# Performance work log

Hardware: AMD Instinct MI355X
Metric: run time of the kernel (lower is better)

## Reference

```python
import jax, jax.numpy as jnp
import numpy as np

NQ = 10          # qubits
NT = 32          # tokens (LCU terms)
DM = 512         # d_model
DEG = 2          # qsvt degree
B = 128          # batch
NPQC = 4 * NQ    # params per PQC application
DIM = 2 ** NQ    # statevector dimension


def ansatz14_spec(q, layers=1):
    spec = []
    for _ in range(layers):
        spec += [('ry', (i,)) for i in range(q)]
        spec += [('crx', (i, (i + 1) % q)) for i in range(q - 1, -1, -1)]
        spec += [('ry', (i,)) for i in range(q)]
        spec += [('crx', (i, (i - 1) % q)) for i in [q - 1] + list(range(q - 1))]
    return spec

SPEC = ansatz14_spec(NQ, 1)


def _gate_ry(theta):
    h = theta * 0.5
    c = jnp.cos(h)
    s = jnp.sin(h)
    m = jnp.stack([jnp.stack([c, -s], -1), jnp.stack([s, c], -1)], -2)
    return m.astype(jnp.complex64)  # (N,2,2)


def _gate_rx(theta):
    h = theta * 0.5
    c = jnp.cos(h).astype(jnp.complex64)
    s = (-1j) * jnp.sin(h).astype(jnp.complex64)
    return jnp.stack([jnp.stack([c, s], -1), jnp.stack([s, c], -1)], -2)


def _apply_1q(state, mats, wire, q):
    # state: (N, 2^q) complex; mats: (N,2,2); wire 0 is most significant bit
    N = state.shape[0]
    a = 2 ** wire
    bdim = 2 ** (q - wire - 1)
    s = state.reshape(N, a, 2, bdim)
    return jnp.einsum('nij,najb->naib', mats, s).reshape(N, 2 ** q)


def _apply_crx(state, theta, c, t, q):
    # controlled-RX: control wire c, target wire t
    N = state.shape[0]
    st = state.reshape((N,) + (2,) * q)
    ax = 1 + c
    s0 = jnp.take(st, 0, axis=ax)   # control = 0 branch: untouched
    s1 = jnp.take(st, 1, axis=ax)   # control = 1 branch: apply RX on target
    tp = t if t < c else t - 1      # target wire position after removing control axis
    s1n = _apply_1q(s1.reshape(N, -1), _gate_rx(theta), tp, q - 1).reshape(s1.shape)
    return jnp.stack([s0, s1n], axis=ax).reshape(N, 2 ** q)


def _apply_pqc(state, params, q):
    # params: (N, NPQC); fixed small gate list -> Python loop is fine
    for k, (fn, w) in enumerate(SPEC):
        th = params[:, k]
        if fn == 'ry':
            state = _apply_1q(state, _gate_ry(th), w[0], q)
        else:
            state = _apply_crx(state, th, w[0], w[1], q)
    return state


def _apply_lcu(states, params, lcu):
    # states: (B, DIM) complex; params: (B, L, NPQC); lcu: (B, L) complex
    Bn, L = lcu.shape
    rep = jnp.repeat(states, L, axis=0)                    # (B*L, DIM)
    st = _apply_pqc(rep, params.reshape(Bn * L, NPQC), NQ)
    return jnp.einsum('bld,bl->bd', st.reshape(Bn, L, DIM), lcu)


def _measure_xyz(state, q):
    # Pauli expectations per wire: order [X_0..X_{q-1}, Y_0.., Z_0..]
    N = state.shape[0]
    xs, ys, zs = [], [], []
    for w in range(q):
        s = state.reshape(N, 2 ** w, 2, -1)
        a0, a1 = s[:, :, 0, :], s[:, :, 1, :]
        cross = jnp.sum(jnp.conj(a0) * a1, axis=(1, 2))
        xs.append(2.0 * jnp.real(cross))
        ys.append(2.0 * jnp.imag(cross))
        zs.append(jnp.sum(jnp.abs(a0) ** 2 - jnp.abs(a1) ** 2, axis=(1, 2)))
    return jnp.stack(xs + ys + zs, axis=1).astype(jnp.float32)  # (B, 3q)


def reference(tokens_emb, W, b, lcu_re, lcu_im, qsvt_coeffs, ff_params):
    Bn, L, D = tokens_emb.shape
    L = min(L, NT)
    pqc_params = tokens_emb[:, :L] @ W.T + b               # (B, L, NPQC)
    lcu = (lcu_re + 1j * lcu_im).astype(jnp.complex64)[:L]
    lcu = lcu / jnp.sum(jnp.abs(lcu))
    lcu_b = jnp.broadcast_to(lcu[None], (Bn, L))
    init = jnp.zeros((Bn, DIM), jnp.complex64).at[:, 0].set(1.0)
    acc = qsvt_coeffs[0].astype(jnp.complex64) * init
    mono = init
    for k in range(1, DEG + 1):
        mono = _apply_lcu(mono, pqc_params, lcu_b)
        acc = acc + qsvt_coeffs[k].astype(jnp.complex64) * mono
    state = acc / jnp.sum(jnp.abs(qsvt_coeffs))
    state = state / jnp.linalg.norm(state, axis=-1, keepdims=True)
    ffp = jnp.broadcast_to(ff_params[None], (Bn, NPQC))
    state = _apply_pqc(state, ffp, NQ)
    return _measure_xyz(state, NQ)


def setup_inputs():
    key = jax.random.key(0)
    ks = jax.random.split(key, 7)
    return {
        'tokens_emb': jax.random.normal(ks[0], (B, NT, DM), jnp.float32),
        'W': jax.random.normal(ks[1], (NPQC, DM), jnp.float32) * 0.05,
        'b': jax.random.normal(ks[2], (NPQC,), jnp.float32),
        'lcu_re': jax.random.normal(ks[3], (NT,), jnp.float32),
        'lcu_im': jax.random.normal(ks[4], (NT,), jnp.float32),
        'qsvt_coeffs': jax.random.normal(ks[5], (DEG + 1,), jnp.float32),
        'ff_params': jax.random.normal(ks[6], (NPQC,), jnp.float32),
    }
```

## Files before the change

### kernel.cpp

```cpp
#include <hip/hip_runtime.h>
#include <hip/hip_bf16.h>


#define NQ   10
#define NT   32
#define DM   512
#define BATCH 128
#define NPQC 40
#define DIM  1024
#define NROWS (BATCH * NT)
#define PSTRIDE (BATCH * DIM)

typedef float v2f __attribute__((ext_vector_type(2)));

#define WAITLDS asm volatile("s_waitcnt lgkmcnt(0)" ::: "memory")

__device__ __forceinline__ v2f Jrot(v2f v) {
  return __builtin_shufflevector(v, -v, 1, 2);
}
__device__ __forceinline__ v2f Jc(v2f v) {
  return __builtin_shufflevector(-v, v, 1, 2);
}


template<int B>
__device__ __forceinline__ void g_ry(v2f (&a)[16], float c, float s) {
  static_assert(B >= 6, "RY targets must be register bits");
  constexpr int m = 1 << (B - 6);
#pragma unroll
  for (int r = 0; r < 16; ++r) {
    if (!(r & m)) {
      int r1 = r | m;
      v2f a0 = a[r], a1 = a[r1];
      a[r]  = c * a0 - s * a1;
      a[r1] = s * a0 + c * a1;
    }
  }
}

template<int BC, int BT>
__device__ __forceinline__ void g_crx(v2f (&a)[16], int lane, float c, float s) {
  static_assert(BT >= 6, "CRX targets must be register bits");
  constexpr int m = 1 << (BT - 6);
  bool lane_ok = (BC >= 6) || ((lane >> BC) & 1);
  float ce = lane_ok ? c : 1.f;
  float se = lane_ok ? s : 0.f;
#pragma unroll
  for (int r = 0; r < 16; ++r) {
    if (!(r & m)) {
      if constexpr (BC >= 6) { if (!((r >> (BC - 6)) & 1)) continue; }
      int r1 = r | m;
      v2f a0 = a[r], a1 = a[r1];
      a[r]  = ce * a0 + se * Jrot(a1);
      a[r1] = ce * a1 + se * Jrot(a0);
    }
  }
}

template<int L0, int L1, int L2, int L3>
__device__ __forceinline__ void remap(v2f (&a)[16], v2f* __restrict__ slab,
                                      int lane) {
  constexpr int LM = (1 << L0) | (1 << L1) | (1 << L2) | (1 << L3);
#pragma unroll
  for (int r = 0; r < 16; ++r) {
    int f = 0;
    if (L0 < 4 && (r & 1)) f |= 1 << L0;
    if (L1 < 4 && (r & 2)) f |= 1 << L1;
    if (L2 < 4 && (r & 4)) f |= 1 << L2;
    if (L3 < 4 && (r & 8)) f |= 1 << L3;
    slab[r * 64 + (lane ^ f)] = a[r];
  }
  WAITLDS;
  int la = lane & ~LM & 63;
  la |= ((lane >> L0) & 1) << 6;
  la |= ((lane >> L1) & 1) << 7;
  la |= ((lane >> L2) & 1) << 8;
  la |= ((lane >> L3) & 1) << 9;
  if (L0 < 4) la |= ((lane >> L0) & 1) << L0;
  if (L1 < 4) la |= ((lane >> L1) & 1) << L1;
  if (L2 < 4) la |= ((lane >> L2) & 1) << L2;
  if (L3 < 4) la |= ((lane >> L3) & 1) << L3;
#pragma unroll
  for (int r = 0; r < 16; ++r) {
    int rc = ((r & 1) ? (1 << L0) : 0) | ((r & 2) ? (1 << L1) : 0)
           | ((r & 4) ? (1 << L2) : 0) | ((r & 8) ? (1 << L3) : 0);
    a[r] = slab[la ^ rc];
  }
}

template<bool SKIP_HEAD>
__device__ __forceinline__ void apply_pqc_phased(v2f (&a)[16],
    const float2* __restrict__ cs, v2f* __restrict__ slab, int lane) {
#define RYt(B, t)      g_ry<B>(a, t.x, t.y);
#define CXt(BC, BT, t) g_crx<BC, BT>(a, lane, t.x, t.y);
  float2 t10 = cs[10], t11 = cs[11], t12 = cs[12];
  if constexpr (!SKIP_HEAD) {
    float2 t0 = cs[0], t1 = cs[1], t2 = cs[2], t3 = cs[3];
    float2 t4 = cs[4], t5 = cs[5], t6 = cs[6], t7 = cs[7];
    float2 t8 = cs[8], t9 = cs[9];
    RYt(9,t0) RYt(8,t1) RYt(7,t2) RYt(6,t3)
    remap<5,4,3,2>(a, slab, lane);
    RYt(6,t4) RYt(7,t5) RYt(8,t6) RYt(9,t7)
    remap<1,0,2,3>(a, slab, lane);
    RYt(6,t8) RYt(7,t9)
  }
  CXt(7,8,t10) CXt(6,7,t11) CXt(3,6,t12)
  float2 t13 = cs[13], t14 = cs[14], t15 = cs[15], t16 = cs[16];
  remap<1,0,2,3>(a, slab, lane);
  CXt(8,9,t13) CXt(7,8,t14) CXt(6,7,t15) CXt(5,6,t16)
  float2 t17 = cs[17], t18 = cs[18], t19 = cs[19];
  float2 t20 = cs[20], t21 = cs[21], t22 = cs[22], t23 = cs[23];
  remap<2,3,4,5>(a, slab, lane);
  CXt(8,9,t17) CXt(7,8,t18) CXt(6,7,t19)
  RYt(6,t20) RYt(7,t21) RYt(8,t22) RYt(9,t23)
  float2 t24 = cs[24], t25 = cs[25], t26 = cs[26], t27 = cs[27];
  remap<2,3,4,5>(a, slab, lane);
  RYt(6,t24) RYt(7,t25) RYt(8,t26) RYt(9,t27)
  float2 t28 = cs[28], t29 = cs[29];
  float2 t30 = cs[30], t31 = cs[31], t32 = cs[32], t33 = cs[33];
  remap<1,0,2,3>(a, slab, lane);
  RYt(6,t28) RYt(7,t29)
  CXt(7,6,t30) CXt(8,7,t31) CXt(9,8,t32) CXt(4,9,t33)
  float2 t34 = cs[34], t35 = cs[35], t36 = cs[36], t37 = cs[37];
  remap<4,5,1,0>(a, slab, lane);
  CXt(7,6,t34) CXt(8,7,t35) CXt(9,8,t36) CXt(2,9,t37)
  float2 t38 = cs[38], t39 = cs[39];
  remap<2,3,4,5>(a, slab, lane);
  CXt(7,6,t38) CXt(8,7,t39)
#undef RYt
#undef CXt
}

__device__ __forceinline__ int p8_lane_canon(int lane) {
  return (((lane >> 1) & 1) << 9) | ((lane & 1) << 8) | (((lane >> 2) & 1) << 7)
       | (((lane >> 3) & 1) << 6) | (((lane >> 4) & 1) << 5) | (((lane >> 5) & 1) << 4);
}

__device__ __forceinline__ void stagger(int key) {
  int s = key & 3;
  if (s & 1) __builtin_amdgcn_s_sleep(1);
  if (s & 2) __builtin_amdgcn_s_sleep(2);
}

__global__ __launch_bounds__(256) void params_kernel(
    const float* __restrict__ emb, const float* __restrict__ W,
    const float* __restrict__ bias,
    const float* __restrict__ lcu_re, const float* __restrict__ lcu_im,
    const float* __restrict__ ffp,
    float2* __restrict__ cs, float2* __restrict__ ffcs, float2* __restrict__ lcu) {
  int blk = blockIdx.x;
  int tid = threadIdx.x;
  if (blk == 256) {
    if (tid < NPQC) {
      float h = 0.5f * ffp[tid];
      ffcs[tid] = make_float2(cosf(h), sinf(h));
    }
    if (tid == 64) {
      float ssum = 0.f;
      for (int i = 0; i < NT; ++i) {
        float re = lcu_re[i], im = lcu_im[i];
        ssum += sqrtf(re * re + im * im);
      }
      float inv = 1.f / ssum;
      for (int i = 0; i < NT; ++i)
        lcu[i] = make_float2(lcu_re[i] * inv, lcu_im[i] * inv);
    }
    return;
  }

  __shared__ float Asl[16 * 516];
  int row0 = blk * 16;

  const float4* eg = (const float4*)(emb + (size_t)row0 * DM);
#pragma unroll
  for (int i = 0; i < 8; ++i) {
    int e = tid + i * 256;
    int r = e >> 7, k4 = e & 127;
    float4 v = eg[e];
    *(float4*)&Asl[r * 516 + k4 * 4] = v;
  }
  __syncthreads();

  int kq = tid >> 6;
  int lane = tid & 63;
  int rg = lane >> 3;
  int cg = lane & 7;

  const float* Ar0 = &Asl[(2 * rg) * 516 + kq * 128];
  const float* Ar1 = Ar0 + 516;
  const float* Bg  = W + (size_t)(5 * cg) * DM + kq * 128;

  float acc[2][5] = {};
#pragma unroll 4
  for (int k = 0; k < 128; k += 4) {
    float4 a0 = *(const float4*)(Ar0 + k);
    float4 a1 = *(const float4*)(Ar1 + k);
#pragma unroll
    for (int j = 0; j < 5; ++j) {
      float4 b = *(const float4*)(Bg + j * DM + k);
      acc[0][j] += a0.x * b.x + a0.y * b.y + a0.z * b.z + a0.w * b.w;
      acc[1][j] += a1.x * b.x + a1.y * b.y + a1.z * b.z + a1.w * b.w;
    }
  }

  __syncthreads();
  float* red = Asl;
#pragma unroll
  for (int i = 0; i < 2; ++i)
#pragma unroll
    for (int j = 0; j < 5; ++j)
      red[kq * 644 + (2 * rg + i) * 40 + 5 * cg + j] = acc[i][j];
  __syncthreads();

  for (int o = tid; o < 640; o += 256) {
    float v = bias[o % 40] + red[o] + red[644 + o] + red[1288 + o] + red[1932 + o];
    float h = 0.5f * v;
    cs[(size_t)blk * 640 + o] = make_float2(cosf(h), sinf(h));
  }
}

template<bool FIRST>
__global__ __launch_bounds__(256) void pqc_step(
    const float2* __restrict__ cs, const float2* __restrict__ lcu,
    const v2f* __restrict__ src, v2f* __restrict__ dst) {
  __shared__ v2f slabs[4][1024];
  int lane = threadIdx.x & 63;
  int wvu = __builtin_amdgcn_readfirstlane(threadIdx.x >> 6);
  int blk = blockIdx.x;
  stagger(blk + wvu);
  int b = blk >> 3, qq = blk & 7;
  int l = qq * 4 + wvu;
  const float2* csrow = cs + (size_t)(b * NT + l) * NPQC;
  v2f* slab = slabs[wvu];

  v2f a[16];
  if constexpr (FIRST) {
    float2 f5 = csrow[5], f4 = csrow[4], f6 = csrow[6], f7 = csrow[7];
    float2 f2 = csrow[2], f3 = csrow[3];
    float2 f8 = csrow[8], f9 = csrow[9], f0 = csrow[0], f1 = csrow[1];
    float lp = ((lane & 1) ? f5.y : f5.x);
    lp *= ((lane & 2) ? f4.y : f4.x);
    lp *= ((lane & 4) ? f6.y : f6.x);
    lp *= ((lane & 8) ? f7.y : f7.x);
    lp *= ((lane & 16) ? f2.y : f2.x);
    lp *= ((lane & 32) ? f3.y : f3.x);
#pragma unroll
    for (int r = 0; r < 16; ++r) {
      float rp = ((r & 1) ? f8.y : f8.x) * ((r & 2) ? f9.y : f9.x)
               * ((r & 4) ? f0.y : f0.x) * ((r & 8) ? f1.y : f1.x);
      a[r].x = lp * rp;
      a[r].y = 0.f;
    }
  } else {
    const v2f* s = src + (size_t)b * DIM;
#pragma unroll
    for (int r = 0; r < 16; ++r) a[r] = s[r * 64 + lane];
  }

  apply_pqc_phased<FIRST>(a, csrow, slab, lane);

  float2 w = lcu[l];
  int pl = p8_lane_canon(lane);
  pl ^= (pl >> 5);
#pragma unroll
  for (int r = 0; r < 16; ++r) {
    int rc = ((r & 1) << 3) | ((r & 2) << 1) | ((r & 4) >> 1) | ((r & 8) >> 3);
    slab[pl ^ rc] = w.x * a[r] + w.y * Jc(a[r]);
  }
  __syncthreads();

  v2f* dst_b = dst + (size_t)(qq * BATCH + b) * DIM;
#pragma unroll
  for (int i = 0; i < 4; ++i) {
    int n = threadIdx.x + i * 256;
    int ph = n ^ (n >> 5);
    v2f sum = slabs[0][ph] + slabs[1][ph] + slabs[2][ph] + slabs[3][ph];
    dst_b[n] = sum;
  }
}


__global__ __launch_bounds__(256) void reduce_slices(v2f* __restrict__ buf) {
  int n = blockIdx.x * 256 + threadIdx.x;
  v2f acc = buf[n];
#pragma unroll
  for (int q = 1; q < 8; ++q) acc += buf[n + q * PSTRIDE];
  buf[n] = acc;
}

__global__ __launch_bounds__(256) void final_reduce(
    const v2f* __restrict__ red1, v2f* __restrict__ part2,
    const float* __restrict__ qsvt) {
  __shared__ float rbuf[4];
  int b = blockIdx.x, tid = threadIdx.x;
  int lane = tid & 63, wv = tid >> 6;
  float q0 = qsvt[0], q1 = qsvt[1], q2 = qsvt[2];
  const v2f* r1 = red1 + (size_t)b * DIM;
  v2f* p2 = part2 + (size_t)b * DIM;

  v2f vals[4];
  float nn = 0.f;
#pragma unroll
  for (int i = 0; i < 4; ++i) {
    int n = tid + i * 256;
    v2f m2 = p2[n];
#pragma unroll
    for (int q = 1; q < 8; ++q) m2 += p2[n + q * PSTRIDE];
    v2f v = q1 * r1[n] + q2 * m2;
    if (n == 0) v.x += q0;
    vals[i] = v;
    nn += v.x * v.x + v.y * v.y;
  }
#pragma unroll
  for (int o = 1; o < 64; o <<= 1) nn += __shfl_xor(nn, o);
  if (lane == 0) rbuf[wv] = nn;
  __syncthreads();
  float inv = 1.f / sqrtf(rbuf[0] + rbuf[1] + rbuf[2] + rbuf[3]);
#pragma unroll
  for (int i = 0; i < 4; ++i) p2[tid + i * 256] = vals[i] * inv;
}

__global__ __launch_bounds__(64, 1) void final_pqc(
    const v2f* __restrict__ state, const float2* __restrict__ ffcs,
    float* __restrict__ out) {
  __shared__ v2f st[1024];
  __shared__ float2 ang[40];
  __shared__ float tb[30 * 65];
  int lane = threadIdx.x;
  int b = blockIdx.x;

  const v2f* s = state + (size_t)b * DIM;
#pragma unroll
  for (int r = 0; r < 16; ++r) {
    int n = r * 64 + lane;
    st[n ^ (n >> 5)] = s[n];
  }
  if (lane < NPQC) ang[lane] = ffcs[lane];
  WAITLDS;

#pragma unroll 1
  for (int k = 0; k < NPQC; ++k) {
    int isCrx, c, t;
    if (k < 10)      { isCrx = 0; t = k;      c = 0; }
    else if (k < 20) { int i = 19 - k; isCrx = 1; c = i; t = (i == 9) ? 0 : i + 1; }
    else if (k < 30) { isCrx = 0; t = k - 20; c = 0; }
    else             { int i = (k == 30) ? 9 : k - 31; isCrx = 1; c = i; t = (i == 0) ? 9 : i - 1; }
    int m  = 1 << (9 - t);
    int cb = 9 - c;
    float2 th = ang[k];
    float cg = th.x, sg = th.y;

    v2f a0[8], a1[8];
    int j0[8], j1[8], en[8];
#pragma unroll
    for (int p = 0; p < 8; ++p) {
      int q  = p * 64 + lane;
      int i0 = ((q & ~(m - 1)) << 1) | (q & (m - 1));
      int i1 = i0 | m;
      j0[p] = i0 ^ (i0 >> 5);
      j1[p] = i1 ^ (i1 >> 5);
      en[p] = (i0 >> cb) & 1;
      a0[p] = st[j0[p]];
      a1[p] = st[j1[p]];
    }
    WAITLDS;
#pragma unroll
    for (int p = 0; p < 8; ++p) {
      v2f n0, n1;
      if (!isCrx) {
        n0 = cg * a0[p] - sg * a1[p];
        n1 = sg * a0[p] + cg * a1[p];
      } else {
        float ce = en[p] ? cg : 1.f;
        float se = en[p] ? sg : 0.f;
        n0 = ce * a0[p] + se * Jrot(a1[p]);
        n1 = ce * a1[p] + se * Jrot(a0[p]);
      }
      st[j0[p]] = n0;
      st[j1[p]] = n1;
    }
    WAITLDS;
  }

#pragma unroll 1
  for (int w = 0; w < NQ; ++w) {
    int m = 1 << (9 - w);
    float xr = 0.f, xi = 0.f, zz = 0.f;
#pragma unroll
    for (int p = 0; p < 8; ++p) {
      int q  = p * 64 + lane;
      int i0 = ((q & ~(m - 1)) << 1) | (q & (m - 1));
      int i1 = i0 | m;
      v2f a0 = st[i0 ^ (i0 >> 5)];
      v2f a1 = st[i1 ^ (i1 >> 5)];
      xr += a0.x * a1.x + a0.y * a1.y;
      xi += a0.x * a1.y - a0.y * a1.x;
      zz += a0.x * a0.x + a0.y * a0.y - a1.x * a1.x - a1.y * a1.y;
    }
    tb[w * 65 + lane]        = xr;
    tb[(10 + w) * 65 + lane] = xi;
    tb[(20 + w) * 65 + lane] = zz;
  }
  WAITLDS;
  if (lane < 30) {
    float s2 = 0.f;
#pragma unroll
    for (int k2 = 0; k2 < 64; ++k2) s2 += tb[lane * 65 + k2];
    float sc = (lane < 20) ? 2.f : 1.f;
    out[b * 30 + lane] = sc * s2;
  }
}


extern "C" void kernel_launch(void* const* d_in, const int* in_sizes, int n_in,
                              void* d_out, int out_size, void* d_ws, size_t ws_size,
                              hipStream_t stream) {
  const float* emb    = (const float*)d_in[0];
  const float* W      = (const float*)d_in[1];
  const float* bias   = (const float*)d_in[2];
  const float* lcu_re = (const float*)d_in[3];
  const float* lcu_im = (const float*)d_in[4];
  const float* qsvt   = (const float*)d_in[5];
  const float* ffp    = (const float*)d_in[6];
  float* out = (float*)d_out;

  char* ws = (char*)d_ws;
  float2* cs    = (float2*)ws;
  float2* ffcs  = (float2*)(ws + 1310720);
  float2* lcu   = (float2*)(ws + 1311040);
  v2f*    part1 = (v2f*)(ws + 1311744);
  v2f*    part2 = (v2f*)(ws + 1311744 + 8388608);

  params_kernel<<<257, 256, 0, stream>>>(emb, W, bias, lcu_re, lcu_im, ffp,
                                         cs, ffcs, lcu);
  pqc_step<true><<<1024, 256, 0, stream>>>(cs, lcu, nullptr, part1);
  reduce_slices<<<512, 256, 0, stream>>>(part1);
  pqc_step<false><<<1024, 256, 0, stream>>>(cs, lcu, part1, part2);
  final_reduce<<<BATCH, 256, 0, stream>>>(part1, part2, qsvt);
  final_pqc<<<BATCH, 64, 0, stream>>>(part2, ffcs, out);
}
```

Before: 166.7 us.

## Fuse final reduce and final PQC into one 256-thread kernel; drop stagger sleeps

After: 151.3 us. 9.2% less time.

```diff
diff --git a/kernel.cpp b/kernel.cpp
--- a/kernel.cpp
+++ b/kernel.cpp
@@ -136,12 +136,6 @@
        | (((lane >> 3) & 1) << 6) | (((lane >> 4) & 1) << 5) | (((lane >> 5) & 1) << 4);
 }
 
-__device__ __forceinline__ void stagger(int key) {
-  int s = key & 3;
-  if (s & 1) __builtin_amdgcn_s_sleep(1);
-  if (s & 2) __builtin_amdgcn_s_sleep(2);
-}
-
 __global__ __launch_bounds__(256) void params_kernel(
     const float* __restrict__ emb, const float* __restrict__ W,
     const float* __restrict__ bias,
@@ -227,7 +221,6 @@
   int lane = threadIdx.x & 63;
   int wvu = __builtin_amdgcn_readfirstlane(threadIdx.x >> 6);
   int blk = blockIdx.x;
-  stagger(blk + wvu);
   int b = blk >> 3, qq = blk & 7;
   int l = qq * 4 + wvu;
   const float2* csrow = cs + (size_t)(b * NT + l) * NPQC;
@@ -288,15 +281,21 @@
   buf[n] = acc;
 }
 
-__global__ __launch_bounds__(256) void final_reduce(
-    const v2f* __restrict__ red1, v2f* __restrict__ part2,
-    const float* __restrict__ qsvt) {
+__global__ __launch_bounds__(256) void final_fused(
+    const v2f* __restrict__ red1, const v2f* __restrict__ part2,
+    const float* __restrict__ qsvt, const float2* __restrict__ ffcs,
+    float* __restrict__ out) {
+  __shared__ v2f st[1024];
+  __shared__ float2 ang[40];
   __shared__ float rbuf[4];
+  __shared__ float tb[30 * 257];
   int b = blockIdx.x, tid = threadIdx.x;
   int lane = tid & 63, wv = tid >> 6;
   float q0 = qsvt[0], q1 = qsvt[1], q2 = qsvt[2];
   const v2f* r1 = red1 + (size_t)b * DIM;
-  v2f* p2 = part2 + (size_t)b * DIM;
+  const v2f* p2 = part2 + (size_t)b * DIM;
+
+  if (tid < NPQC) ang[tid] = ffcs[tid];
 
   v2f vals[4];
   float nn = 0.f;
@@ -317,26 +316,11 @@
   __syncthreads();
   float inv = 1.f / sqrtf(rbuf[0] + rbuf[1] + rbuf[2] + rbuf[3]);
 #pragma unroll
-  for (int i = 0; i < 4; ++i) p2[tid + i * 256] = vals[i] * inv;
-}
-
-__global__ __launch_bounds__(64, 1) void final_pqc(
-    const v2f* __restrict__ state, const float2* __restrict__ ffcs,
-    float* __restrict__ out) {
-  __shared__ v2f st[1024];
-  __shared__ float2 ang[40];
-  __shared__ float tb[30 * 65];
-  int lane = threadIdx.x;
-  int b = blockIdx.x;
-
-  const v2f* s = state + (size_t)b * DIM;
-#pragma unroll
-  for (int r = 0; r < 16; ++r) {
-    int n = r * 64 + lane;
-    st[n ^ (n >> 5)] = s[n];
-  }
-  if (lane < NPQC) ang[lane] = ffcs[lane];
-  WAITLDS;
+  for (int i = 0; i < 4; ++i) {
+    int n = tid + i * 256;
+    st[n ^ (n >> 5)] = vals[i] * inv;
+  }
+  __syncthreads();
 
 #pragma unroll 1
   for (int k = 0; k < NPQC; ++k) {
@@ -350,11 +334,11 @@
     float2 th = ang[k];
     float cg = th.x, sg = th.y;
 
-    v2f a0[8], a1[8];
-    int j0[8], j1[8], en[8];
-#pragma unroll
-    for (int p = 0; p < 8; ++p) {
-      int q  = p * 64 + lane;
+    v2f a0[2], a1[2];
+    int j0[2], j1[2], en[2];
+#pragma unroll
+    for (int p = 0; p < 2; ++p) {
+      int q  = p * 256 + tid;
       int i0 = ((q & ~(m - 1)) << 1) | (q & (m - 1));
       int i1 = i0 | m;
       j0[p] = i0 ^ (i0 >> 5);
@@ -363,9 +347,8 @@
       a0[p] = st[j0[p]];
       a1[p] = st[j1[p]];
     }
-    WAITLDS;
-#pragma unroll
-    for (int p = 0; p < 8; ++p) {
+#pragma unroll
+    for (int p = 0; p < 2; ++p) {
       v2f n0, n1;
       if (!isCrx) {
         n0 = cg * a0[p] - sg * a1[p];
@@ -379,7 +362,7 @@
       st[j0[p]] = n0;
       st[j1[p]] = n1;
     }
-    WAITLDS;
+    __syncthreads();
   }
 
 #pragma unroll 1
@@ -387,8 +370,8 @@
     int m = 1 << (9 - w);
     float xr = 0.f, xi = 0.f, zz = 0.f;
 #pragma unroll
-    for (int p = 0; p < 8; ++p) {
-      int q  = p * 64 + lane;
+    for (int p = 0; p < 2; ++p) {
+      int q  = p * 256 + tid;
       int i0 = ((q & ~(m - 1)) << 1) | (q & (m - 1));
       int i1 = i0 | m;
       v2f a0 = st[i0 ^ (i0 >> 5)];
@@ -397,17 +380,17 @@
       xi += a0.x * a1.y - a0.y * a1.x;
       zz += a0.x * a0.x + a0.y * a0.y - a1.x * a1.x - a1.y * a1.y;
     }
-    tb[w * 65 + lane]        = xr;
-    tb[(10 + w) * 65 + lane] = xi;
-    tb[(20 + w) * 65 + lane] = zz;
-  }
-  WAITLDS;
-  if (lane < 30) {
+    tb[w * 257 + tid]        = xr;
+    tb[(10 + w) * 257 + tid] = xi;
+    tb[(20 + w) * 257 + tid] = zz;
+  }
+  __syncthreads();
+  if (tid < 30) {
     float s2 = 0.f;
-#pragma unroll
-    for (int k2 = 0; k2 < 64; ++k2) s2 += tb[lane * 65 + k2];
-    float sc = (lane < 20) ? 2.f : 1.f;
-    out[b * 30 + lane] = sc * s2;
+#pragma unroll 8
+    for (int t = 0; t < 256; ++t) s2 += tb[tid * 257 + t];
+    float sc = (tid < 20) ? 2.f : 1.f;
+    out[b * 30 + tid] = sc * s2;
   }
 }
 
@@ -436,6 +419,5 @@
   pqc_step<true><<<1024, 256, 0, stream>>>(cs, lcu, nullptr, part1);
   reduce_slices<<<512, 256, 0, stream>>>(part1);
   pqc_step<false><<<1024, 256, 0, stream>>>(cs, lcu, part1, part2);
-  final_reduce<<<BATCH, 256, 0, stream>>>(part1, part2, qsvt);
-  final_pqc<<<BATCH, 64, 0, stream>>>(part2, ffcs, out);
-}
+  final_fused<<<BATCH, 256, 0, stream>>>(part1, part2, qsvt, ffcs, out);
+}
```
